# Performance work log

Hardware: AMD Instinct MI355X
Metric: run time of the kernel (lower is better)

The kernel has to match this reference:

```python
import jax, jax.numpy as jnp
import numpy as np

D_MODEL = 1024
D_STATE = 16
D_CONV = 4
EXPAND = 2
D_INNER = EXPAND * D_MODEL          # 2048
DT_RANK = (D_MODEL + 15) // 16      # 64
EPS = 1e-5
BATCH, SEQ = 2, 1024


def setup_inputs() -> dict:
    key = jax.random.key(0)
    ks = jax.random.split(key, 10)
    s = 0.02
    x = jax.random.normal(ks[0], (BATCH, SEQ, D_MODEL), jnp.float32)
    norm_w = jnp.ones((D_MODEL,), jnp.float32)
    in_proj_w = jax.random.normal(ks[1], (2 * D_INNER, D_MODEL), jnp.float32) * s
    conv_w = jax.random.normal(ks[2], (D_INNER, D_CONV), jnp.float32) * 0.2
    conv_b = jnp.zeros((D_INNER,), jnp.float32)
    x_proj_w = jax.random.normal(ks[3], (DT_RANK + 2 * D_STATE, D_INNER), jnp.float32) * s
    dt_proj_w = jax.random.normal(ks[4], (D_INNER, DT_RANK), jnp.float32) * s
    dt_proj_b = jnp.full((D_INNER,), -2.0, jnp.float32)  # softplus(-2) ~ 0.127, realistic dt init
    # S4D-real init: A[d, n] = n+1  => A_log = log(1..N)
    A_log = jnp.log(jnp.broadcast_to(jnp.arange(1, D_STATE + 1, dtype=jnp.float32), (D_INNER, D_STATE)))
    D = jnp.ones((D_INNER,), jnp.float32)
    out_proj_w = jax.random.normal(ks[5], (D_MODEL, D_INNER), jnp.float32) * s
    return dict(x=x, norm_w=norm_w, in_proj_w=in_proj_w, conv_w=conv_w, conv_b=conv_b,
                x_proj_w=x_proj_w, dt_proj_w=dt_proj_w, dt_proj_b=dt_proj_b,
                A_log=A_log, D=D, out_proj_w=out_proj_w)


def _mamba_forward(x, norm_w, in_proj_w, conv_w, conv_b, x_proj_w,
                   dt_proj_w, dt_proj_b, A_log, D, out_proj_w):
    # Block: residual = x ; h = RMSNorm(residual) ; out = Mamba(h)
    residual = x
    h = x * jax.lax.rsqrt(jnp.mean(x * x, axis=-1, keepdims=True) + EPS) * norm_w

    # in_proj -> split into (xc, z), each [B, L, D_INNER]
    xz = jnp.einsum('bld,ed->ble', h, in_proj_w)
    xc, z = jnp.split(xz, 2, axis=-1)

    # causal depthwise conv1d (kernel D_CONV) + SiLU
    xp = jnp.pad(xc, ((0, 0), (D_CONV - 1, 0), (0, 0)))
    conv = conv_b
    for k in range(D_CONV):  # tiny fixed loop over kernel taps
        conv = conv + conv_w[:, k] * xp[:, k:k + SEQ, :]
    xs = jax.nn.silu(conv)  # [B, L, D_INNER]

    # x_proj -> dt, B_t, C_t
    x_dbl = jnp.einsum('bld,ed->ble', xs, x_proj_w)
    dt_r = x_dbl[..., :DT_RANK]
    B_t = x_dbl[..., DT_RANK:DT_RANK + D_STATE]           # [B, L, N]
    C_t = x_dbl[..., DT_RANK + D_STATE:]                  # [B, L, N]
    dt = jax.nn.softplus(jnp.einsum('blr,dr->bld', dt_r, dt_proj_w) + dt_proj_b)  # [B, L, D_INNER]

    # selective scan: h_t = exp(dt*A) h_{t-1} + dt * B_t * u_t ; y_t = C_t . h_t + D u_t
    A = -jnp.exp(A_log)                                   # [D_INNER, N]
    deltaA = jnp.exp(dt[..., None] * A)                   # [B, L, D_INNER, N]
    deltaBu = (dt * xs)[..., None] * B_t[:, :, None, :]   # [B, L, D_INNER, N]

    def combine(e1, e2):
        a1, b1 = e1
        a2, b2 = e2
        return a1 * a2, a2 * b1 + b2

    _, hstates = jax.lax.associative_scan(combine, (deltaA, deltaBu), axis=1)
    y = jnp.einsum('bldn,bln->bld', hstates, C_t) + D * xs
    y = y * jax.nn.silu(z)
    out = jnp.einsum('bld,ed->ble', y, out_proj_w)

    # MambaBlock: y = mixer_out + residual
    return out + residual


def reference(x, norm_w, in_proj_w, conv_w, conv_b, x_proj_w,
              dt_proj_w, dt_proj_b, A_log, D, out_proj_w):
    return _mamba_forward(x, norm_w, in_proj_w, conv_w, conv_b, x_proj_w,
                          dt_proj_w, dt_proj_b, A_log, D, out_proj_w)
```

## Files before the change

### kernel.cpp

```cpp
#include <hip/hip_runtime.h>
#include <hip/hip_bf16.h>


#define BATCH 2
#define SEQ 1024
#define DMODEL 1024
#define DINNER 2048
#define DTRANK 64
#define DSTATE 16
#define NROWS (BATCH * SEQ)
#define NC 32
#define CL (SEQ / NC)
#define NSPLIT 8
#define KCH (DINNER / NSPLIT)

typedef __bf16 bf16_t;
typedef __bf16 bf16x2 __attribute__((ext_vector_type(2)));
typedef __bf16 bf16x4 __attribute__((ext_vector_type(4)));
typedef __bf16 bf16x8 __attribute__((ext_vector_type(8)));
typedef float f32x4 __attribute__((ext_vector_type(4)));

#define GLOAD_LDS16(gp, lp)                                              \
    __builtin_amdgcn_global_load_lds(                                    \
        (const __attribute__((address_space(1))) void*)(gp),             \
        (__attribute__((address_space(3))) void*)(lp), 16, 0, 0)

__global__ __launch_bounds__(256) void k_prep(
    const float* __restrict__ x, const float* __restrict__ w,
    bf16_t* __restrict__ h,
    const float* __restrict__ s0, bf16_t* __restrict__ d0,
    const float* __restrict__ s1, bf16_t* __restrict__ d1,
    const float* __restrict__ s2, bf16_t* __restrict__ d2)
{
    const int tid = threadIdx.x;
    if (blockIdx.x < NROWS) {
        const int row = blockIdx.x;
        const float* xr = x + (size_t)row * DMODEL;
        float4 xv = *(const float4*)(xr + tid * 4);
        float s = xv.x * xv.x + xv.y * xv.y + xv.z * xv.z + xv.w * xv.w;
#pragma unroll
        for (int m = 1; m <= 32; m <<= 1) s += __shfl_xor(s, m, 64);
        __shared__ float red[4];
        if ((tid & 63) == 0) red[tid >> 6] = s;
        __syncthreads();
        float tot = red[0] + red[1] + red[2] + red[3];
        float scale = rsqrtf(tot * (1.0f / DMODEL) + 1e-5f);
        float4 wv = *(const float4*)(w + tid * 4);
        bf16x4 hv;
        hv.x = (bf16_t)(xv.x * scale * wv.x);
        hv.y = (bf16_t)(xv.y * scale * wv.y);
        hv.z = (bf16_t)(xv.z * scale * wv.z);
        hv.w = (bf16_t)(xv.w * scale * wv.w);
        *(bf16x4*)(h + (size_t)row * DMODEL + tid * 4) = hv;
        return;
    }
    const int i = (blockIdx.x - NROWS) * 256 + tid;
    const float* src; bf16_t* dst; int off;
    if (i < 1048576) { src = s0; dst = d0; off = i; }
    else if (i < 1048576 + 524288) { src = s1; dst = d1; off = i - 1048576; }
    else { src = s2; dst = d2; off = i - 1048576 - 524288; }
    float4 v = *(const float4*)(src + (size_t)off * 4);
    bf16x4 o;
    o.x = (bf16_t)v.x; o.y = (bf16_t)v.y; o.z = (bf16_t)v.z; o.w = (bf16_t)v.w;
    *(bf16x4*)(dst + (size_t)off * 4) = o;
}

template <int BM, int BN, bool BF16_OUT>
__global__ __launch_bounds__(256) void k_gemm_db(
    const bf16_t* __restrict__ A,
    const bf16_t* __restrict__ W,
    void* __restrict__ Cv, int ldc,
    const float* __restrict__ resid,
    int K)
{
    constexpr int NGA = BM / 32;
    constexpr int NGB = BN / 32;
    constexpr int MF = BM / 32;
    constexpr int NF = BN / 32;

    __shared__ __align__(16) bf16_t lA[2][BM * 64];
    __shared__ __align__(16) bf16_t lB[2][BN * 64];

    const int tid = threadIdx.x;
    const int wave = tid >> 6;
    const int lane = tid & 63;

    const int nbx = gridDim.x;
    const int lin = blockIdx.y * nbx + blockIdx.x;
    const int chunk = (nbx * gridDim.y) >> 3;
    const int wid = (lin & 7) * chunk + (lin >> 3);
    const int m0 = (wid % nbx) * BM;
    const int n0 = (wid / nbx) * BN;

    const int wm = (wave >> 1) * (BM / 2);
    const int wn = (wave & 1) * (BN / 2);
    const int fr = lane & 15;
    const int fg = lane >> 4;

    const bf16_t* ga[NGA];
    const bf16_t* gb[NGB];
    int lofA[NGA], lofB[NGB];
#pragma unroll
    for (int g = 0; g < NGA; ++g) {
        const int gi = g * 256 + tid;
        const int row = gi >> 3;
        const int col = (gi & 7) ^ (row & 7);
        ga[g] = A + (size_t)(m0 + row) * K + col * 8;
        lofA[g] = (g * 256 + wave * 64) * 8;
    }
#pragma unroll
    for (int g = 0; g < NGB; ++g) {
        const int gi = g * 256 + tid;
        const int row = gi >> 3;
        const int col = (gi & 7) ^ (row & 7);
        gb[g] = W + (size_t)(n0 + row) * K + col * 8;
        lofB[g] = (g * 256 + wave * 64) * 8;
    }

    f32x4 acc[MF][NF] = {};

#pragma unroll
    for (int g = 0; g < NGA; ++g) GLOAD_LDS16(ga[g], lA[0] + lofA[g]);
#pragma unroll
    for (int g = 0; g < NGB; ++g) GLOAD_LDS16(gb[g], lB[0] + lofB[g]);

    for (int k0 = 0; k0 < K; k0 += 64) {
        const int p = (k0 >> 6) & 1;
        const bool more = (k0 + 64) < K;
        __syncthreads();
        if (more) {
#pragma unroll
            for (int g = 0; g < NGA; ++g)
                GLOAD_LDS16(ga[g] + (k0 + 64), lA[p ^ 1] + lofA[g]);
#pragma unroll
            for (int g = 0; g < NGB; ++g)
                GLOAD_LDS16(gb[g] + (k0 + 64), lB[p ^ 1] + lofB[g]);
        }
#pragma unroll
        for (int s = 0; s < 2; ++s) {
            bf16x8 af[MF], bf[NF];
#pragma unroll
            for (int i = 0; i < MF; ++i) {
                const int rr = wm + i * 16 + fr;
                af[i] = *(const bf16x8*)(lA[p] + (size_t)(rr * 8 + ((s * 4 + fg) ^ (rr & 7))) * 8);
            }
#pragma unroll
            for (int j = 0; j < NF; ++j) {
                const int rr = wn + j * 16 + fr;
                bf[j] = *(const bf16x8*)(lB[p] + (size_t)(rr * 8 + ((s * 4 + fg) ^ (rr & 7))) * 8);
            }
#pragma unroll
            for (int i = 0; i < MF; ++i)
#pragma unroll
                for (int j = 0; j < NF; ++j)
                    acc[i][j] = __builtin_amdgcn_mfma_f32_16x16x32_bf16(
                        af[i], bf[j], acc[i][j], 0, 0, 0);
        }
    }

#pragma unroll
    for (int i = 0; i < MF; ++i) {
        const int rbase = m0 + wm + i * 16 + (lane >> 4) * 4;
#pragma unroll
        for (int rr = 0; rr < 4; ++rr) {
            const int row = rbase + rr;
            if (BF16_OUT) {
                bf16_t* cr = (bf16_t*)Cv + (size_t)row * ldc;
#pragma unroll
                for (int j = 0; j < NF; ++j)
                    cr[n0 + wn + j * 16 + fr] = (bf16_t)acc[i][j][rr];
            } else {
                float* cr = (float*)Cv + (size_t)row * ldc;
                const float* ar = resid + (size_t)row * ldc;
#pragma unroll
                for (int j = 0; j < NF; ++j) {
                    const int col = n0 + wn + j * 16 + fr;
                    cr[col] = acc[i][j][rr] + ar[col];
                }
            }
        }
    }
}

#define XBK 16
__global__ __launch_bounds__(256) void k_gemm_xproj(
    const bf16_t* __restrict__ xz,
    const float* __restrict__ cw,
    const float* __restrict__ cb,
    const float* __restrict__ W,
    float* __restrict__ part,
    bf16_t* __restrict__ xsout)
{
    __shared__ __align__(16) float As[2][XBK][36];
    __shared__ __align__(16) float Ws[2][XBK][100];
    __shared__ float cwL[KCH * 4];
    __shared__ float cbL[KCH];
    const int tid = threadIdx.x;
    const int m0 = blockIdx.x * 32;
    const int kbase = blockIdx.y * KCH;

    const int ar = tid >> 3;
    const int ac = (tid & 7) << 1;
    const int wr = tid >> 2;
    const int wk = (tid & 3) << 2;
    const int tm = tid >> 4;
    const int tn = tid & 15;

    const int l = m0 + ar;
    const int lloc = l & (SEQ - 1);

    {
        float4 v = *(const float4*)(cw + (size_t)kbase * 4 + tid * 4);
        *(float4*)&cwL[tid * 4] = v;
        cbL[tid] = cb[kbase + tid];
    }

    auto stage_load = [&](int kq, bf16x2 (&xv)[4], float4& wv0, float4& wv1) {
#pragma unroll
        for (int kk = 0; kk < 4; ++kk) {
            bf16x2 z = {};
            xv[kk] = z;
            if (lloc - 3 + kk >= 0)
                xv[kk] = *(const bf16x2*)(xz + (size_t)(l - 3 + kk) * (2 * DINNER)
                                          + kbase + kq + ac);
        }
        wv0 = *(const float4*)(W + (size_t)wr * DINNER + kbase + kq + wk);
        if (tid < 128)
            wv1 = *(const float4*)(W + (size_t)(64 + wr) * DINNER + kbase + kq + wk);
    };

    auto stage_write = [&](int kq, int pbuf, const bf16x2 (&xv)[4],
                           const float4& wv0, const float4& wv1) {
        const int e = kq + ac;
        float s0 = cbL[e], s1 = cbL[e + 1];
#pragma unroll
        for (int kk = 0; kk < 4; ++kk) {
            s0 = fmaf(cwL[(e + 0) * 4 + kk], (float)xv[kk].x, s0);
            s1 = fmaf(cwL[(e + 1) * 4 + kk], (float)xv[kk].y, s1);
        }
        s0 = s0 / (1.0f + __expf(-s0));
        s1 = s1 / (1.0f + __expf(-s1));
        As[pbuf][ac + 0][ar] = s0;
        As[pbuf][ac + 1][ar] = s1;
        bf16x2 o;
        o.x = (bf16_t)s0; o.y = (bf16_t)s1;
        *(bf16x2*)(xsout + (size_t)l * DINNER + kbase + e) = o;
        Ws[pbuf][wk + 0][wr] = wv0.x;
        Ws[pbuf][wk + 1][wr] = wv0.y;
        Ws[pbuf][wk + 2][wr] = wv0.z;
        Ws[pbuf][wk + 3][wr] = wv0.w;
        if (tid < 128) {
            Ws[pbuf][wk + 0][64 + wr] = wv1.x;
            Ws[pbuf][wk + 1][64 + wr] = wv1.y;
            Ws[pbuf][wk + 2][64 + wr] = wv1.z;
            Ws[pbuf][wk + 3][64 + wr] = wv1.w;
        }
    };

    __syncthreads();

    {
        bf16x2 xv[4]; float4 wv0 = {}, wv1 = {};
        stage_load(0, xv, wv0, wv1);
        stage_write(0, 0, xv, wv0, wv1);
    }

    float acc[2][6] = {};
    constexpr int NSTEP = KCH / XBK;

    for (int ks = 0; ks < NSTEP; ++ks) {
        const int p = ks & 1;
        __syncthreads();
        const bool more = (ks + 1) < NSTEP;
        bf16x2 xv[4]; float4 wv0 = {}, wv1 = {};
        if (more) stage_load((ks + 1) * XBK, xv, wv0, wv1);

#pragma unroll
        for (int kk = 0; kk < XBK; ++kk) {
            const float2 av  = *(const float2*)&As[p][kk][tm * 2];
            const float2 w01 = *(const float2*)&Ws[p][kk][tn * 6 + 0];
            const float2 w23 = *(const float2*)&Ws[p][kk][tn * 6 + 2];
            const float2 w45 = *(const float2*)&Ws[p][kk][tn * 6 + 4];
            acc[0][0] = fmaf(av.x, w01.x, acc[0][0]);
            acc[1][0] = fmaf(av.y, w01.x, acc[1][0]);
            acc[0][1] = fmaf(av.x, w01.y, acc[0][1]);
            acc[1][1] = fmaf(av.y, w01.y, acc[1][1]);
            acc[0][2] = fmaf(av.x, w23.x, acc[0][2]);
            acc[1][2] = fmaf(av.y, w23.x, acc[1][2]);
            acc[0][3] = fmaf(av.x, w23.y, acc[0][3]);
            acc[1][3] = fmaf(av.y, w23.y, acc[1][3]);
            acc[0][4] = fmaf(av.x, w45.x, acc[0][4]);
            acc[1][4] = fmaf(av.y, w45.x, acc[1][4]);
            acc[0][5] = fmaf(av.x, w45.y, acc[0][5]);
            acc[1][5] = fmaf(av.y, w45.y, acc[1][5]);
        }
        if (more) stage_write((ks + 1) * XBK, p ^ 1, xv, wv0, wv1);
    }

    float* pb = part + (size_t)blockIdx.y * NROWS * 96;
#pragma unroll
    for (int i = 0; i < 2; ++i) {
        float* pr = pb + (size_t)(m0 + tm * 2 + i) * 96 + tn * 6;
#pragma unroll
        for (int j = 0; j < 6; ++j) pr[j] = acc[i][j];
    }
}

__global__ __launch_bounds__(256) void k_xproj_reduce(
    const float* __restrict__ part, float* __restrict__ xdbl,
    bf16_t* __restrict__ dtr)
{
    const int idx = blockIdx.x * 256 + threadIdx.x;
    if (idx >= NROWS * 24) return;
    const int row = idx / 24;
    const int c4 = (idx % 24) * 4;
    f32x4 s = {0.f, 0.f, 0.f, 0.f};
#pragma unroll
    for (int p = 0; p < NSPLIT; ++p)
        s += *(const f32x4*)(part + (size_t)p * NROWS * 96 + (size_t)row * 96 + c4);
    *(f32x4*)(xdbl + (size_t)row * 96 + c4) = s;
    if (c4 < 64) {
        bf16x4 o;
        o.x = (bf16_t)s.x; o.y = (bf16_t)s.y; o.z = (bf16_t)s.z; o.w = (bf16_t)s.w;
        *(bf16x4*)(dtr + (size_t)row * 64 + c4) = o;
    }
}

__device__ __forceinline__ void dtproj_tile(
    const bf16_t* __restrict__ dtr, const bf16_t* __restrict__ dtw,
    bf16_t* __restrict__ sDT, int trow0, int d0, int tid)
{
    const int wv = tid >> 6;
    const int ln = tid & 63;
    const int fr = ln & 15;
    const int fg = ln >> 4;
#pragma unroll
    for (int mt = 0; mt < 2; ++mt) {
        const bf16x8 a0 = *(const bf16x8*)(dtr + (size_t)(trow0 + mt * 16 + fr) * 64 + fg * 8);
        const bf16x8 a1 = *(const bf16x8*)(dtr + (size_t)(trow0 + mt * 16 + fr) * 64 + 32 + fg * 8);
#pragma unroll
        for (int j = 0; j < 4; ++j) {
            const int drow = d0 + wv * 64 + j * 16 + fr;
            const bf16x8 b0 = *(const bf16x8*)(dtw + (size_t)drow * 64 + fg * 8);
            const bf16x8 b1 = *(const bf16x8*)(dtw + (size_t)drow * 64 + 32 + fg * 8);
            f32x4 acc = {0.f, 0.f, 0.f, 0.f};
            acc = __builtin_amdgcn_mfma_f32_16x16x32_bf16(a0, b0, acc, 0, 0, 0);
            acc = __builtin_amdgcn_mfma_f32_16x16x32_bf16(a1, b1, acc, 0, 0, 0);
            const int tl = mt * 16 + fg * 4;
            const int dl = wv * 64 + j * 16 + fr;
#pragma unroll
            for (int r = 0; r < 4; ++r)
                sDT[(tl + r) * 256 + dl] = (bf16_t)acc[r];
        }
    }
}

__global__ __launch_bounds__(256) void k_scan_sum(
    const bf16_t* __restrict__ dtr, const bf16_t* __restrict__ dtw,
    const float* __restrict__ dtb,
    const bf16_t* __restrict__ xs, const float* __restrict__ xdbl,
    float* __restrict__ Qpb, float* __restrict__ sloc)
{
    const int tid = threadIdx.x;
    const int g = blockIdx.x & 7;
    const int c = (blockIdx.x >> 3) & (NC - 1);
    const int b = blockIdx.x >> 8;
    const int d0 = g * 256;
    const int d = d0 + tid;

    __shared__ __align__(16) bf16_t sDT[CL * 256];
    __shared__ __align__(16) bf16_t sXS[CL * 256];
    __shared__ float sB[CL * 16];
    {
        const int t = tid >> 4, n = tid & 15;
#pragma unroll
        for (int tt = 0; tt < CL; tt += 16)
            sB[(t + tt) * 16 + n] =
                xdbl[(size_t)(b * SEQ + c * CL + t + tt) * 96 + 64 + n];
    }
#pragma unroll
    for (int i = 0; i < 4; ++i) {
        const int gi = i * 256 + tid;
        const int t = gi >> 5;
        const int c8 = (gi & 31) * 8;
        const size_t ga = (size_t)(b * SEQ + c * CL + t) * DINNER + d0 + c8;
        *(bf16x8*)(sXS + t * 256 + c8) = *(const bf16x8*)(xs + ga);
    }
    dtproj_tile(dtr, dtw, sDT, b * SEQ + c * CL, d0, tid);

    float st[16];
#pragma unroll
    for (int n = 0; n < 16; ++n) st[n] = 0.0f;
    float P = 1.0f;
    const float bias = dtb[d];
    __syncthreads();

    for (int t = 0; t < CL; ++t) {
        const float dlv = (float)sDT[t * 256 + tid] + bias;
        const float dtv = (dlv > 20.0f) ? dlv : __logf(1.0f + __expf(dlv));
        const float du = dtv * (float)sXS[t * 256 + tid];
        const float q = __expf(-dtv);
        P *= q;
        float a = q;
#pragma unroll
        for (int n4 = 0; n4 < 4; ++n4) {
            const f32x4 Bv = *(const f32x4*)&sB[t * 16 + n4 * 4];
#pragma unroll
            for (int j = 0; j < 4; ++j) {
                st[n4 * 4 + j] = a * st[n4 * 4 + j] + du * Bv[j];
                a *= q;
            }
        }
    }
    Qpb[(size_t)(b * NC + c) * DINNER + d] = P;
#pragma unroll
    for (int n = 0; n < 16; ++n)
        sloc[((size_t)((b * NC + c) * 16 + n)) * DINNER + d] = st[n];
}

__global__ __launch_bounds__(256) void k_scan_combine(
    const float* __restrict__ Qpb, const float* __restrict__ sloc,
    float* __restrict__ hinit)
{
    const int tid = threadIdx.x;
    const int g = blockIdx.x & 7;
    const int n = (blockIdx.x >> 3) & 15;
    const int b = blockIdx.x >> 7;
    const int d = g * 256 + tid;
    float h = 0.0f;
    for (int c = 0; c < NC; ++c) {
        const size_t i16 = ((size_t)((b * NC + c) * 16 + n)) * DINNER + d;
        hinit[i16] = h;
        const float Q = Qpb[(size_t)(b * NC + c) * DINNER + d];
        float Qn = Q;
        for (int i = 0; i < n; ++i) Qn *= Q;
        h = Qn * h + sloc[i16];
    }
}

__global__ __launch_bounds__(256) void k_scan_out(
    const bf16_t* __restrict__ dtr, const bf16_t* __restrict__ dtw,
    const float* __restrict__ dtb,
    const bf16_t* __restrict__ xs, const float* __restrict__ xdbl,
    const bf16_t* __restrict__ xz, const float* __restrict__ Dp,
    const float* __restrict__ hinit,
    bf16_t* __restrict__ yg)
{
    const int tid = threadIdx.x;
    const int g = blockIdx.x & 7;
    const int c = (blockIdx.x >> 3) & (NC - 1);
    const int b = blockIdx.x >> 8;
    const int d0 = g * 256;
    const int d = d0 + tid;

    __shared__ __align__(16) bf16_t sDT[CL * 256];
    __shared__ __align__(16) bf16_t sXS[CL * 256];
    __shared__ __align__(16) bf16_t sZ[CL * 256];
    __shared__ float sB[CL * 16];
    __shared__ float sC[CL * 16];
    {
        const int t = tid >> 4, n = tid & 15;
#pragma unroll
        for (int tt = 0; tt < CL; tt += 16) {
            const size_t base = (size_t)(b * SEQ + c * CL + t + tt) * 96;
            sB[(t + tt) * 16 + n] = xdbl[base + 64 + n];
            sC[(t + tt) * 16 + n] = xdbl[base + 80 + n];
        }
    }
#pragma unroll
    for (int i = 0; i < 4; ++i) {
        const int gi = i * 256 + tid;
        const int t = gi >> 5;
        const int c8 = (gi & 31) * 8;
        const int row = b * SEQ + c * CL + t;
        const size_t ga = (size_t)row * DINNER + d0 + c8;
        *(bf16x8*)(sXS + t * 256 + c8) = *(const bf16x8*)(xs + ga);
        *(bf16x8*)(sZ + t * 256 + c8) =
            *(const bf16x8*)(xz + (size_t)row * (2 * DINNER) + DINNER + d0 + c8);
    }
    dtproj_tile(dtr, dtw, sDT, b * SEQ + c * CL, d0, tid);

    float st[16];
#pragma unroll
    for (int n = 0; n < 16; ++n)
        st[n] = hinit[((size_t)((b * NC + c) * 16 + n)) * DINNER + d];
    const float bias = dtb[d];
    const float Dd = Dp[d];
    __syncthreads();

    for (int t = 0; t < CL; ++t) {
        const float dlv = (float)sDT[t * 256 + tid] + bias;
        const float dtv = (dlv > 20.0f) ? dlv : __logf(1.0f + __expf(dlv));
        const float xv = (float)sXS[t * 256 + tid];
        const float du = dtv * xv;
        const float q = __expf(-dtv);
        float a = q;
        float part = 0.0f;
#pragma unroll
        for (int n4 = 0; n4 < 4; ++n4) {
            const f32x4 Bv = *(const f32x4*)&sB[t * 16 + n4 * 4];
            const f32x4 Cw = *(const f32x4*)&sC[t * 16 + n4 * 4];
#pragma unroll
            for (int j = 0; j < 4; ++j) {
                const int n = n4 * 4 + j;
                st[n] = a * st[n] + du * Bv[j];
                part = fmaf(st[n], Cw[j], part);
                a *= q;
            }
        }
        const float zv = (float)sZ[t * 256 + tid];
        const float sig = 1.0f / (1.0f + __expf(-zv));
        yg[(size_t)(b * SEQ + c * CL + t) * DINNER + d] =
            (bf16_t)((part + Dd * xv) * (zv * sig));
    }
}

extern "C" void kernel_launch(void* const* d_in, const int* in_sizes, int n_in,
                              void* d_out, int out_size, void* d_ws, size_t ws_size,
                              hipStream_t stream) {
    const float* x = (const float*)d_in[0];
    const float* norm_w = (const float*)d_in[1];
    const float* in_proj_w = (const float*)d_in[2];
    const float* conv_w = (const float*)d_in[3];
    const float* conv_b = (const float*)d_in[4];
    const float* x_proj_w = (const float*)d_in[5];
    const float* dt_proj_b = (const float*)d_in[7];
    const float* Dp = (const float*)d_in[9];
    const float* out_proj_w = (const float*)d_in[10];
    const float* dt_proj_w = (const float*)d_in[6];
    float* out = (float*)d_out;

    char* ws = (char*)d_ws;
    bf16_t* xz    = (bf16_t*)(ws);
    bf16_t* xsb   = (bf16_t*)(ws + 16777216);
    float*  xdbl  = (float*) (ws + 25165824);
    float*  sloc  = (float*) (ws + 34340864);
    float*  Qpb   = (float*) (ws + 42729472);
    float*  hinit = (float*) (ws + 43253760);
    bf16_t* ygb   = (bf16_t*)(ws + 51642368);
    bf16_t* hb    = (bf16_t*)(ws + 60030976);
    bf16_t* inw   = (bf16_t*)(ws + 64225280);
    bf16_t* outw  = (bf16_t*)(ws + 72613888);
    bf16_t* dtw   = (bf16_t*)(ws + 76808192);
    bf16_t* dtr   = (bf16_t*)(ws + 77070336);
    float*  xpart = (float*) (ws + 77332480);

    k_prep<<<NROWS + 6272, 256, 0, stream>>>(x, norm_w, hb,
                                             in_proj_w, inw,
                                             out_proj_w, outw,
                                             dt_proj_w, dtw);

    {
        dim3 g(NROWS / 128, (2 * DINNER) / 128);
        k_gemm_db<128, 128, true><<<g, 256, 0, stream>>>(hb, inw, xz, 2 * DINNER,
                                                         nullptr, DMODEL);
    }

    {
        dim3 g(NROWS / 32, NSPLIT);
        k_gemm_xproj<<<g, 256, 0, stream>>>(xz, conv_w, conv_b, x_proj_w,
                                            xpart, xsb);
    }
    k_xproj_reduce<<<(NROWS * 24 + 255) / 256, 256, 0, stream>>>(xpart, xdbl, dtr);

    k_scan_sum<<<BATCH * NC * 8, 256, 0, stream>>>(dtr, dtw, dt_proj_b, xsb,
                                                   xdbl, Qpb, sloc);
    k_scan_combine<<<BATCH * DSTATE * 8, 256, 0, stream>>>(Qpb, sloc, hinit);
    k_scan_out<<<BATCH * NC * 8, 256, 0, stream>>>(dtr, dtw, dt_proj_b, xsb,
                                                   xdbl, xz, Dp, hinit, ygb);

    {
        dim3 g(NROWS / 64, DMODEL / 64);
        k_gemm_db<64, 64, false><<<g, 256, 0, stream>>>(ygb, outw, out, DMODEL,
                                                        x, DINNER);
    }
}
```

Before: 227.2 us.

## Fuse xproj reduce and three scan kernels into one cooperative kernel

Measured after the change: 527.8 us. 2.32x slower.

```diff
diff --git a/kernel.cpp b/kernel.cpp
--- a/kernel.cpp
+++ b/kernel.cpp
@@ -1,5 +1,6 @@
 #include <hip/hip_runtime.h>
 #include <hip/hip_bf16.h>
+#include <hip/hip_cooperative_groups.h>
 
 
 #define BATCH 2
@@ -13,6 +14,8 @@
 #define CL (SEQ / NC)
 #define NSPLIT 8
 #define KCH (DINNER / NSPLIT)
+
+namespace cg = cooperative_groups;
 
 typedef __bf16 bf16_t;
 typedef __bf16 bf16x2 __attribute__((ext_vector_type(2)));
@@ -306,26 +309,6 @@
     }
 }
 
-__global__ __launch_bounds__(256) void k_xproj_reduce(
-    const float* __restrict__ part, float* __restrict__ xdbl,
-    bf16_t* __restrict__ dtr)
-{
-    const int idx = blockIdx.x * 256 + threadIdx.x;
-    if (idx >= NROWS * 24) return;
-    const int row = idx / 24;
-    const int c4 = (idx % 24) * 4;
-    f32x4 s = {0.f, 0.f, 0.f, 0.f};
-#pragma unroll
-    for (int p = 0; p < NSPLIT; ++p)
-        s += *(const f32x4*)(part + (size_t)p * NROWS * 96 + (size_t)row * 96 + c4);
-    *(f32x4*)(xdbl + (size_t)row * 96 + c4) = s;
-    if (c4 < 64) {
-        bf16x4 o;
-        o.x = (bf16_t)s.x; o.y = (bf16_t)s.y; o.z = (bf16_t)s.z; o.w = (bf16_t)s.w;
-        *(bf16x4*)(dtr + (size_t)row * 64 + c4) = o;
-    }
-}
-
 __device__ __forceinline__ void dtproj_tile(
     const bf16_t* __restrict__ dtr, const bf16_t* __restrict__ dtw,
     bf16_t* __restrict__ sDT, int trow0, int d0, int tid)
@@ -355,101 +338,46 @@
     }
 }
 
-__global__ __launch_bounds__(256) void k_scan_sum(
-    const bf16_t* __restrict__ dtr, const bf16_t* __restrict__ dtw,
+__global__ __launch_bounds__(256) void k_scan_fused(
+    const float* __restrict__ part,
+    float* __restrict__ xdbl,
+    bf16_t* __restrict__ dtr,
+    const bf16_t* __restrict__ dtw,
     const float* __restrict__ dtb,
-    const bf16_t* __restrict__ xs, const float* __restrict__ xdbl,
-    float* __restrict__ Qpb, float* __restrict__ sloc)
-{
-    const int tid = threadIdx.x;
-    const int g = blockIdx.x & 7;
-    const int c = (blockIdx.x >> 3) & (NC - 1);
-    const int b = blockIdx.x >> 8;
-    const int d0 = g * 256;
-    const int d = d0 + tid;
-
-    __shared__ __align__(16) bf16_t sDT[CL * 256];
-    __shared__ __align__(16) bf16_t sXS[CL * 256];
-    __shared__ float sB[CL * 16];
-    {
-        const int t = tid >> 4, n = tid & 15;
-#pragma unroll
-        for (int tt = 0; tt < CL; tt += 16)
-            sB[(t + tt) * 16 + n] =
-                xdbl[(size_t)(b * SEQ + c * CL + t + tt) * 96 + 64 + n];
-    }
-#pragma unroll
-    for (int i = 0; i < 4; ++i) {
-        const int gi = i * 256 + tid;
-        const int t = gi >> 5;
-        const int c8 = (gi & 31) * 8;
-        const size_t ga = (size_t)(b * SEQ + c * CL + t) * DINNER + d0 + c8;
-        *(bf16x8*)(sXS + t * 256 + c8) = *(const bf16x8*)(xs + ga);
-    }
-    dtproj_tile(dtr, dtw, sDT, b * SEQ + c * CL, d0, tid);
-
-    float st[16];
-#pragma unroll
-    for (int n = 0; n < 16; ++n) st[n] = 0.0f;
-    float P = 1.0f;
-    const float bias = dtb[d];
-    __syncthreads();
-
-    for (int t = 0; t < CL; ++t) {
-        const float dlv = (float)sDT[t * 256 + tid] + bias;
-        const float dtv = (dlv > 20.0f) ? dlv : __logf(1.0f + __expf(dlv));
-        const float du = dtv * (float)sXS[t * 256 + tid];
-        const float q = __expf(-dtv);
-        P *= q;
-        float a = q;
-#pragma unroll
-        for (int n4 = 0; n4 < 4; ++n4) {
-            const f32x4 Bv = *(const f32x4*)&sB[t * 16 + n4 * 4];
-#pragma unroll
-            for (int j = 0; j < 4; ++j) {
-                st[n4 * 4 + j] = a * st[n4 * 4 + j] + du * Bv[j];
-                a *= q;
-            }
-        }
-    }
-    Qpb[(size_t)(b * NC + c) * DINNER + d] = P;
-#pragma unroll
-    for (int n = 0; n < 16; ++n)
-        sloc[((size_t)((b * NC + c) * 16 + n)) * DINNER + d] = st[n];
-}
-
-__global__ __launch_bounds__(256) void k_scan_combine(
-    const float* __restrict__ Qpb, const float* __restrict__ sloc,
-    float* __restrict__ hinit)
-{
-    const int tid = threadIdx.x;
-    const int g = blockIdx.x & 7;
-    const int n = (blockIdx.x >> 3) & 15;
-    const int b = blockIdx.x >> 7;
-    const int d = g * 256 + tid;
-    float h = 0.0f;
-    for (int c = 0; c < NC; ++c) {
-        const size_t i16 = ((size_t)((b * NC + c) * 16 + n)) * DINNER + d;
-        hinit[i16] = h;
-        const float Q = Qpb[(size_t)(b * NC + c) * DINNER + d];
-        float Qn = Q;
-        for (int i = 0; i < n; ++i) Qn *= Q;
-        h = Qn * h + sloc[i16];
-    }
-}
-
-__global__ __launch_bounds__(256) void k_scan_out(
-    const bf16_t* __restrict__ dtr, const bf16_t* __restrict__ dtw,
-    const float* __restrict__ dtb,
-    const bf16_t* __restrict__ xs, const float* __restrict__ xdbl,
-    const bf16_t* __restrict__ xz, const float* __restrict__ Dp,
-    const float* __restrict__ hinit,
+    const bf16_t* __restrict__ xs,
+    const bf16_t* __restrict__ xz,
+    const float* __restrict__ Dp,
+    float* __restrict__ Qpb, float* __restrict__ sloc,
+    float* __restrict__ hinit,
     bf16_t* __restrict__ yg)
 {
     const int tid = threadIdx.x;
-    const int g = blockIdx.x & 7;
-    const int c = (blockIdx.x >> 3) & (NC - 1);
-    const int b = blockIdx.x >> 8;
+    const int bid = blockIdx.x;
+    cg::grid_group grid = cg::this_grid();
+
+    {
+        const int idx = bid * 256 + tid;
+        if (idx < NROWS * 24) {
+            const int row = idx / 24;
+            const int c4 = (idx % 24) * 4;
+            f32x4 s = {0.f, 0.f, 0.f, 0.f};
+#pragma unroll
+            for (int p = 0; p < NSPLIT; ++p)
+                s += *(const f32x4*)(part + (size_t)p * NROWS * 96 + (size_t)row * 96 + c4);
+            *(f32x4*)(xdbl + (size_t)row * 96 + c4) = s;
+            if (c4 < 64) {
+                bf16x4 o;
+                o.x = (bf16_t)s.x; o.y = (bf16_t)s.y; o.z = (bf16_t)s.z; o.w = (bf16_t)s.w;
+                *(bf16x4*)(dtr + (size_t)row * 64 + c4) = o;
+            }
+        }
+    }
+    __threadfence();
+    grid.sync();
+
+    const int g = bid & 7;
+    const int c = (bid >> 3) & (NC - 1);
+    const int b = bid >> 8;
     const int d0 = g * 256;
     const int d = d0 + tid;
 
@@ -458,6 +386,7 @@
     __shared__ __align__(16) bf16_t sZ[CL * 256];
     __shared__ float sB[CL * 16];
     __shared__ float sC[CL * 16];
+
     {
         const int t = tid >> 4, n = tid & 15;
 #pragma unroll
@@ -482,11 +411,58 @@
 
     float st[16];
 #pragma unroll
+    for (int n = 0; n < 16; ++n) st[n] = 0.0f;
+    float P = 1.0f;
+    const float bias = dtb[d];
+    __syncthreads();
+
+    for (int t = 0; t < CL; ++t) {
+        const float dlv = (float)sDT[t * 256 + tid] + bias;
+        const float dtv = (dlv > 20.0f) ? dlv : __logf(1.0f + __expf(dlv));
+        const float du = dtv * (float)sXS[t * 256 + tid];
+        const float q = __expf(-dtv);
+        P *= q;
+        float a = q;
+#pragma unroll
+        for (int n4 = 0; n4 < 4; ++n4) {
+            const f32x4 Bv = *(const f32x4*)&sB[t * 16 + n4 * 4];
+#pragma unroll
+            for (int j = 0; j < 4; ++j) {
+                st[n4 * 4 + j] = a * st[n4 * 4 + j] + du * Bv[j];
+                a *= q;
+            }
+        }
+    }
+    Qpb[(size_t)(b * NC + c) * DINNER + d] = P;
+#pragma unroll
+    for (int n = 0; n < 16; ++n)
+        sloc[((size_t)((b * NC + c) * 16 + n)) * DINNER + d] = st[n];
+
+    __threadfence();
+    grid.sync();
+
+    if (bid < 256) {
+        const int gg = bid & 7;
+        const int nn = (bid >> 3) & 15;
+        const int bb = bid >> 7;
+        const int dd = gg * 256 + tid;
+        float h = 0.0f;
+        for (int cc = 0; cc < NC; ++cc) {
+            const size_t i16 = ((size_t)((bb * NC + cc) * 16 + nn)) * DINNER + dd;
+            hinit[i16] = h;
+            const float Q = Qpb[(size_t)(bb * NC + cc) * DINNER + dd];
+            float Qn = Q;
+            for (int i = 0; i < nn; ++i) Qn *= Q;
+            h = Qn * h + sloc[i16];
+        }
+    }
+    __threadfence();
+    grid.sync();
+
+#pragma unroll
     for (int n = 0; n < 16; ++n)
         st[n] = hinit[((size_t)((b * NC + c) * 16 + n)) * DINNER + d];
-    const float bias = dtb[d];
     const float Dd = Dp[d];
-    __syncthreads();
 
     for (int t = 0; t < CL; ++t) {
         const float dlv = (float)sDT[t * 256 + tid] + bias;
@@ -495,7 +471,7 @@
         const float du = dtv * xv;
         const float q = __expf(-dtv);
         float a = q;
-        float part = 0.0f;
+        float part3 = 0.0f;
 #pragma unroll
         for (int n4 = 0; n4 < 4; ++n4) {
             const f32x4 Bv = *(const f32x4*)&sB[t * 16 + n4 * 4];
@@ -504,14 +480,14 @@
             for (int j = 0; j < 4; ++j) {
                 const int n = n4 * 4 + j;
                 st[n] = a * st[n] + du * Bv[j];
-                part = fmaf(st[n], Cw[j], part);
+                part3 = fmaf(st[n], Cw[j], part3);
                 a *= q;
             }
         }
         const float zv = (float)sZ[t * 256 + tid];
         const float sig = 1.0f / (1.0f + __expf(-zv));
         yg[(size_t)(b * SEQ + c * CL + t) * DINNER + d] =
-            (bf16_t)((part + Dd * xv) * (zv * sig));
+            (bf16_t)((part3 + Dd * xv) * (zv * sig));
     }
 }
 
@@ -524,10 +500,10 @@
     const float* conv_w = (const float*)d_in[3];
     const float* conv_b = (const float*)d_in[4];
     const float* x_proj_w = (const float*)d_in[5];
+    const float* dt_proj_w = (const float*)d_in[6];
     const float* dt_proj_b = (const float*)d_in[7];
     const float* Dp = (const float*)d_in[9];
     const float* out_proj_w = (const float*)d_in[10];
-    const float* dt_proj_w = (const float*)d_in[6];
     float* out = (float*)d_out;
 
     char* ws = (char*)d_ws;
@@ -561,13 +537,16 @@
         k_gemm_xproj<<<g, 256, 0, stream>>>(xz, conv_w, conv_b, x_proj_w,
                                             xpart, xsb);
     }
-    k_xproj_reduce<<<(NROWS * 24 + 255) / 256, 256, 0, stream>>>(xpart, xdbl, dtr);
-
-    k_scan_sum<<<BATCH * NC * 8, 256, 0, stream>>>(dtr, dtw, dt_proj_b, xsb,
-                                                   xdbl, Qpb, sloc);
-    k_scan_combine<<<BATCH * DSTATE * 8, 256, 0, stream>>>(Qpb, sloc, hinit);
-    k_scan_out<<<BATCH * NC * 8, 256, 0, stream>>>(dtr, dtw, dt_proj_b, xsb,
-                                                   xdbl, xz, Dp, hinit, ygb);
+
+    {
+        void* args[] = {
+            (void*)&xpart, (void*)&xdbl, (void*)&dtr, (void*)&dtw,
+            (void*)&dt_proj_b, (void*)&xsb, (void*)&xz, (void*)&Dp,
+            (void*)&Qpb, (void*)&sloc, (void*)&hinit, (void*)&ygb
+        };
+        hipLaunchCooperativeKernel((void*)k_scan_fused, dim3(512), dim3(256),
+                                   args, 0, stream);
+    }
 
     {
         dim3 g(NROWS / 64, DMODEL / 64);
```
